# Performance work log

Hardware: AMD Instinct MI355X
Metric: run time of the kernel (lower is better)

## Reference

```python
import jax, jax.numpy as jnp
import numpy as np

NUM_NODES = 200000
NUM_EDGES = 600000
NUM_GRAPHS = 10000
BN_EPS = 1e-5


def setup_inputs() -> dict:
    key = jax.random.key(0)
    ks = jax.random.split(key, 10)
    x = jax.random.normal(ks[0], (NUM_NODES, 78), dtype=jnp.float32)
    edge_index = jax.random.randint(ks[1], (2, NUM_EDGES), 0, NUM_NODES, dtype=jnp.int64 if jax.config.jax_enable_x64 else jnp.int32)
    batch = jnp.sort(jax.random.randint(ks[2], (NUM_NODES,), 0, NUM_GRAPHS))
    def glorot(k, shape):
        fan_in, fan_out = shape[-2], shape[-1]
        s = jnp.sqrt(2.0 / (fan_in + fan_out))
        return jax.random.normal(k, shape, dtype=jnp.float32) * s
    return {
        "x": x,
        "edge_index": edge_index,
        "batch": batch,
        "W1_0": glorot(ks[3], (78, 128)),
        "b1_0": jnp.zeros((128,), jnp.float32),
        "W2_0": glorot(ks[4], (128, 128)),
        "b2_0": jnp.zeros((128,), jnp.float32),
        "g_0": jnp.ones((128,), jnp.float32),
        "be_0": jnp.zeros((128,), jnp.float32),
        "W1s": glorot(ks[5], (4, 128, 128)),
        "b1s": jnp.zeros((4, 128), jnp.float32),
        "W2s": glorot(ks[6], (4, 128, 128)),
        "b2s": jnp.zeros((4, 128), jnp.float32),
        "gs": jnp.ones((4, 128), jnp.float32),
        "bes": jnp.zeros((4, 128), jnp.float32),
        "fcW": glorot(ks[7], (128, 64)),
        "fcb": jnp.zeros((64,), jnp.float32),
    }


def _batchnorm(h, gamma, beta):
    # BatchNorm1d with batch statistics (training-mode normalization)
    mean = h.mean(axis=0)
    var = h.var(axis=0)  # biased, as torch uses for normalization
    return gamma * (h - mean) * jax.lax.rsqrt(var + BN_EPS) + beta


def _gin_block(h, src, dst, W1, b1, W2, b2, gamma, beta):
    # GINConv (eps=0): MLP(x + sum of neighbor messages), then ReLU + BN
    agg = jax.ops.segment_sum(h[src], dst, num_segments=NUM_NODES)  # [N, d]
    z = h + agg
    z = jax.nn.relu(z @ W1 + b1) @ W2 + b2
    z = jax.nn.relu(z)
    return _batchnorm(z, gamma, beta)


def reference(x, edge_index, batch, W1_0, b1_0, W2_0, b2_0, g_0, be_0,
              W1s, b1s, W2s, b2s, gs, bes, fcW, fcb):
    src, dst = edge_index[0], edge_index[1]
    h = _gin_block(x, src, dst, W1_0, b1_0, W2_0, b2_0, g_0, be_0)  # [N, 128]

    def body(h, params):
        W1, b1, W2, b2, g, be = params
        return _gin_block(h, src, dst, W1, b1, W2, b2, g, be), None

    h, _ = jax.lax.scan(body, h, (W1s, b1s, W2s, b2s, gs, bes))

    pooled = jax.ops.segment_sum(h, batch, num_segments=NUM_GRAPHS)  # [G, 128]
    out = jax.nn.relu(pooled @ fcW + fcb)  # [G, 64]; dropout is identity at eval
    return out
```

## Files before the change

### kernel.cpp

```cpp
#include <hip/hip_runtime.h>
#include <hip/hip_bf16.h>

#define NN 200000
#define NE 600000
#define NG 10000
#define NCH 98

typedef __attribute__((ext_vector_type(8))) short bfrag;
typedef __attribute__((ext_vector_type(4))) float f32x4;
typedef unsigned short u16;

static __device__ __forceinline__ u16 f2b(float x) {
  __hip_bfloat16 b = __float2bfloat16(x);
  return __builtin_bit_cast(u16, b);
}
static __device__ __forceinline__ float b2f(u16 u) {
  __hip_bfloat16 b = __builtin_bit_cast(__hip_bfloat16, u);
  return __bfloat162float(b);
}
static __device__ __forceinline__ void split(float v, u16& hi, u16& lo) {
  hi = f2b(v);
  lo = f2b(v - b2f(hi));
}

__global__ void prep_kernel(const float* __restrict__ W1_0, const float* __restrict__ W2_0,
                            const float* __restrict__ W1s, const float* __restrict__ W2s,
                            u16* __restrict__ wf) {
  int i = blockIdx.x * 256 + threadIdx.x;
  if (i >= 312 * 64) return;
  int t = i >> 6, lane = i & 63;
  const float* W;
  int KS, ct, kk, Krows, base, half;
  if (t < 24) {
    W = W1_0; KS = 3; ct = t / 3; kk = t - ct * 3; Krows = 78; base = 0; half = 12288;
  } else if (t < 56) {
    int u = t - 24;
    W = W2_0; KS = 4; ct = u >> 2; kk = u & 3; Krows = 128; base = 24576; half = 16384;
  } else {
    int u = t - 56;
    int j = u >> 6, r = u & 63;
    KS = 4; Krows = 128; half = 16384;
    if (r < 32) {
      W = W1s + j * 16384; ct = r >> 2; kk = r & 3; base = 57344 + j * 65536;
    } else {
      W = W2s + j * 16384; r -= 32; ct = r >> 2; kk = r & 3; base = 57344 + j * 65536 + 32768;
    }
  }
  int col = ct * 16 + (lane & 15);
  int idx = ((ct * KS + kk) * 64 + lane) * 8;
  for (int jj = 0; jj < 8; jj++) {
    int k = kk * 32 + 8 * (lane >> 4) + jj;
    float v = (k < Krows) ? W[k * 128 + col] : 0.f;
    u16 hi, lo;
    split(v, hi, lo);
    wf[base + idx + jj] = hi;
    wf[base + half + idx + jj] = lo;
  }
}

__global__ void hist_kernel(const int* __restrict__ dst, int* __restrict__ deg) {
  int e = blockIdx.x * 256 + threadIdx.x;
  if (e < NE) atomicAdd(&deg[dst[e]], 1);
}

__global__ void scan1_kernel(const int* __restrict__ deg, int* __restrict__ csum) {
  __shared__ int s[256];
  int base = blockIdx.x * 2048 + threadIdx.x * 8;
  int t = 0;
#pragma unroll
  for (int j = 0; j < 8; j++) {
    int idx = base + j;
    if (idx < NN) t += deg[idx];
  }
  s[threadIdx.x] = t;
  __syncthreads();
  for (int o = 128; o > 0; o >>= 1) {
    if (threadIdx.x < o) s[threadIdx.x] += s[threadIdx.x + o];
    __syncthreads();
  }
  if (threadIdx.x == 0) csum[blockIdx.x] = s[0];
}

__global__ void scan2_kernel(int* __restrict__ csum, int* __restrict__ rowptr) {
  int acc = 0;
  for (int i = 0; i < NCH; i++) {
    int v = csum[i];
    csum[i] = acc;
    acc += v;
  }
  rowptr[NN] = acc;
}

__global__ void scan3_kernel(const int* deg, const int* __restrict__ csum,
                             int* __restrict__ rowptr, int* cursor) {
  __shared__ int s[256];
  int tid = threadIdx.x;
  int base = blockIdx.x * 2048 + tid * 8;
  int loc[8];
  int t = 0;
#pragma unroll
  for (int j = 0; j < 8; j++) {
    int idx = base + j;
    int d = (idx < NN) ? deg[idx] : 0;
    loc[j] = t;
    t += d;
  }
  s[tid] = t;
  __syncthreads();
  for (int o = 1; o < 256; o <<= 1) {
    int u = (tid >= o) ? s[tid - o] : 0;
    __syncthreads();
    s[tid] += u;
    __syncthreads();
  }
  int off = csum[blockIdx.x] + s[tid] - t;
#pragma unroll
  for (int j = 0; j < 8; j++) {
    int idx = base + j;
    if (idx < NN) {
      int r = off + loc[j];
      rowptr[idx] = r;
      cursor[idx] = r;
    }
  }
}

__global__ void scatter_kernel(const int* __restrict__ src, const int* __restrict__ dst,
                               int* __restrict__ cursor, int* __restrict__ csr_src) {
  int e = blockIdx.x * 256 + threadIdx.x;
  if (e < NE) {
    int p = atomicAdd(&cursor[dst[e]], 1);
    csr_src[p] = src[e];
  }
}

template <bool FIRST>
__global__ __launch_bounds__(512, 4) void fused_kernel(
    const float* __restrict__ xin, const float* __restrict__ hin,
    const float* __restrict__ ss,
    const int* __restrict__ rowptr, const int* __restrict__ csr_src,
    const u16* __restrict__ w1hi, const u16* __restrict__ w1lo,
    const u16* __restrict__ w2hi, const u16* __restrict__ w2lo,
    const float* __restrict__ b1, const float* __restrict__ b2,
    float* __restrict__ hout, float* __restrict__ stats) {
  constexpr int KS1 = FIRST ? 3 : 4;
  constexpr int AH = 0, AL = 8704, TH = 17408, TL = 26112;
  __shared__ u16 lds[34816];
  const int tid = threadIdx.x;
  const int w = tid >> 6, l = tid & 63;
  const int l15 = l & 15, lg = l >> 4;
  const float bb1 = b1[w * 16 + l15];
  const float bb2 = b2[w * 16 + l15];
  float s_acc = 0.f, q_acc = 0.f;

  float4 sc4, sh4;
  if (!FIRST) {
    int k4 = (l & 31) * 4;
    sc4 = *reinterpret_cast<const float4*>(&ss[k4]);
    sh4 = *reinterpret_cast<const float4*>(&ss[128 + k4]);
  }

  for (int tile = blockIdx.x; tile < 3125; tile += gridDim.x) {
    const int rows0 = tile * 64;

    if (FIRST) {
      const float2* x2 = reinterpret_cast<const float2*>(xin);
      for (int j = 0; j < 8; j++) {
        int row = w * 8 + j;
        int node = rows0 + row;
        int beg = rowptr[node], end = rowptr[node + 1];
        int f0 = l * 2;
        if (f0 < 78) {
          size_t fid = (size_t)node * 39 + (f0 >> 1);
          float2 acc = x2[fid];
          int i = beg;
          for (; i + 1 < end; i += 2) {
            int s0 = csr_src[i], s1 = csr_src[i + 1];
            float2 v0 = x2[(size_t)s0 * 39 + (f0 >> 1)];
            float2 v1 = x2[(size_t)s1 * 39 + (f0 >> 1)];
            acc.x += v0.x + v1.x;
            acc.y += v0.y + v1.y;
          }
          if (i < end) {
            int s0 = csr_src[i];
            float2 v0 = x2[(size_t)s0 * 39 + (f0 >> 1)];
            acc.x += v0.x;
            acc.y += v0.y;
          }
          ushort2 oh, ol;
          split(acc.x, oh.x, ol.x);
          split(acc.y, oh.y, ol.y);
          *reinterpret_cast<ushort2*>(&lds[AH + row * 136 + f0]) = oh;
          *reinterpret_cast<ushort2*>(&lds[AL + row * 136 + f0]) = ol;
        } else if (f0 < 96) {
          ushort2 z = {0, 0};
          *reinterpret_cast<ushort2*>(&lds[AH + row * 136 + f0]) = z;
          *reinterpret_cast<ushort2*>(&lds[AL + row * 136 + f0]) = z;
        }
      }
    } else {
      const float4* h4p = reinterpret_cast<const float4*>(hin);
      int k4 = (l & 31) * 4;
      for (int p = 0; p < 4; p++) {
        int row = w * 8 + p * 2 + (l >> 5);
        int node = rows0 + row;
        int beg = rowptr[node], end = rowptr[node + 1];
        size_t foff = (size_t)(k4 >> 2);
        float4 acc = h4p[(size_t)node * 32 + foff];
        int i = beg;
        for (; i + 1 < end; i += 2) {
          int s0 = csr_src[i], s1 = csr_src[i + 1];
          float4 v0 = h4p[(size_t)s0 * 32 + foff];
          float4 v1 = h4p[(size_t)s1 * 32 + foff];
          acc.x += v0.x + v1.x;
          acc.y += v0.y + v1.y;
          acc.z += v0.z + v1.z;
          acc.w += v0.w + v1.w;
        }
        if (i < end) {
          int s0 = csr_src[i];
          float4 v0 = h4p[(size_t)s0 * 32 + foff];
          acc.x += v0.x;
          acc.y += v0.y;
          acc.z += v0.z;
          acc.w += v0.w;
        }
        float cnt = (float)(end - beg + 1);
        float a0 = acc.x * sc4.x + cnt * sh4.x;
        float a1 = acc.y * sc4.y + cnt * sh4.y;
        float a2 = acc.z * sc4.z + cnt * sh4.z;
        float a3 = acc.w * sc4.w + cnt * sh4.w;
        ushort4 oh, ol;
        split(a0, oh.x, ol.x);
        split(a1, oh.y, ol.y);
        split(a2, oh.z, ol.z);
        split(a3, oh.w, ol.w);
        *reinterpret_cast<ushort4*>(&lds[AH + row * 136 + k4]) = oh;
        *reinterpret_cast<ushort4*>(&lds[AL + row * 136 + k4]) = ol;
      }
    }
    bfrag w1h[KS1], w1l[KS1];
#pragma unroll
    for (int kk = 0; kk < KS1; kk++) {
      int fi = ((w * KS1 + kk) * 64 + l) * 8;
      w1h[kk] = *reinterpret_cast<const bfrag*>(&w1hi[fi]);
      w1l[kk] = *reinterpret_cast<const bfrag*>(&w1lo[fi]);
    }
    __syncthreads();

#pragma unroll
    for (int rt = 0; rt < 4; rt++) {
      f32x4 acc = {bb1, bb1, bb1, bb1};
      const int arow = (rt * 16 + l15) * 136 + 8 * lg;
#pragma unroll
      for (int kk = 0; kk < KS1; kk++) {
        bfrag ah = *reinterpret_cast<const bfrag*>(&lds[AH + arow + kk * 32]);
        bfrag al = *reinterpret_cast<const bfrag*>(&lds[AL + arow + kk * 32]);
        acc = __builtin_amdgcn_mfma_f32_16x16x32_bf16(al, w1h[kk], acc, 0, 0, 0);
        acc = __builtin_amdgcn_mfma_f32_16x16x32_bf16(ah, w1l[kk], acc, 0, 0, 0);
        acc = __builtin_amdgcn_mfma_f32_16x16x32_bf16(ah, w1h[kk], acc, 0, 0, 0);
      }
#pragma unroll
      for (int r = 0; r < 4; r++) {
        float v = fmaxf(acc[r], 0.f);
        u16 hi, lo;
        split(v, hi, lo);
        int off = (rt * 16 + 4 * lg + r) * 136 + w * 16 + l15;
        lds[TH + off] = hi;
        lds[TL + off] = lo;
      }
    }
    bfrag w2h[4], w2l[4];
#pragma unroll
    for (int kk = 0; kk < 4; kk++) {
      int fi = ((w * 4 + kk) * 64 + l) * 8;
      w2h[kk] = *reinterpret_cast<const bfrag*>(&w2hi[fi]);
      w2l[kk] = *reinterpret_cast<const bfrag*>(&w2lo[fi]);
    }
    __syncthreads();

#pragma unroll
    for (int rt = 0; rt < 4; rt++) {
      f32x4 acc = {bb2, bb2, bb2, bb2};
      const int arow = (rt * 16 + l15) * 136 + 8 * lg;
#pragma unroll
      for (int kk = 0; kk < 4; kk++) {
        bfrag th = *reinterpret_cast<const bfrag*>(&lds[TH + arow + kk * 32]);
        bfrag tl = *reinterpret_cast<const bfrag*>(&lds[TL + arow + kk * 32]);
        acc = __builtin_amdgcn_mfma_f32_16x16x32_bf16(tl, w2h[kk], acc, 0, 0, 0);
        acc = __builtin_amdgcn_mfma_f32_16x16x32_bf16(th, w2l[kk], acc, 0, 0, 0);
        acc = __builtin_amdgcn_mfma_f32_16x16x32_bf16(th, w2h[kk], acc, 0, 0, 0);
      }
#pragma unroll
      for (int r = 0; r < 4; r++) {
        float v = fmaxf(acc[r], 0.f);
        hout[(size_t)(rows0 + rt * 16 + 4 * lg + r) * 128 + w * 16 + l15] = v;
        s_acc += v;
        q_acc += v * v;
      }
    }
    __syncthreads();
  }
  s_acc += __shfl_xor(s_acc, 16);
  s_acc += __shfl_xor(s_acc, 32);
  q_acc += __shfl_xor(q_acc, 16);
  q_acc += __shfl_xor(q_acc, 32);
  if (lg == 0) {
    atomicAdd(&stats[w * 16 + l15], s_acc);
    atomicAdd(&stats[128 + w * 16 + l15], q_acc);
  }
}

__global__ void bn_kernel(const float* __restrict__ stats, const float* __restrict__ gamma,
                          const float* __restrict__ beta, float* __restrict__ ss) {
  int c = threadIdx.x;
  float mean = stats[c] * (1.f / NN);
  float var = stats[128 + c] * (1.f / NN) - mean * mean;
  var = fmaxf(var, 0.f);
  float sc = gamma[c] * rsqrtf(var + 1e-5f);
  ss[c] = sc;
  ss[128 + c] = beta[c] - mean * sc;
}

__global__ void pool_kernel(const float* __restrict__ h, const float* __restrict__ ss,
                            const int* __restrict__ batch, float* __restrict__ pooled) {
  int c = threadIdx.x;
  int n0 = blockIdx.x * 128;
  int n1 = min(n0 + 128, NN);
  float sc = ss[c], sh = ss[128 + c];
  float acc = 0.f;
  float cnt = 0.f;
  int gprev = batch[n0];
  for (int n = n0; n < n1; n++) {
    int g = batch[n];
    if (g != gprev) {
      atomicAdd(&pooled[gprev * 128 + c], sc * acc + cnt * sh);
      acc = 0.f;
      cnt = 0.f;
      gprev = g;
    }
    acc += h[(size_t)n * 128 + c];
    cnt += 1.f;
  }
  atomicAdd(&pooled[gprev * 128 + c], sc * acc + cnt * sh);
}

__global__ void fc_kernel(const float* __restrict__ pooled, const float* __restrict__ fcW,
                          const float* __restrict__ fcb, float* __restrict__ out) {
  int i = blockIdx.x * 256 + threadIdx.x;
  if (i >= NG * 64) return;
  int g = i >> 6, o = i & 63;
  float acc = fcb[o];
#pragma unroll 8
  for (int k = 0; k < 128; k++) acc += pooled[g * 128 + k] * fcW[k * 64 + o];
  out[i] = fmaxf(acc, 0.f);
}

extern "C" void kernel_launch(void* const* d_in, const int* in_sizes, int n_in,
                              void* d_out, int out_size, void* d_ws, size_t ws_size,
                              hipStream_t stream) {
  const float* x = (const float*)d_in[0];
  const int* ei = (const int*)d_in[1];
  const int* src = ei;
  const int* dst = ei + NE;
  const int* batch = (const int*)d_in[2];
  const float* W1_0 = (const float*)d_in[3];
  const float* b1_0 = (const float*)d_in[4];
  const float* W2_0 = (const float*)d_in[5];
  const float* b2_0 = (const float*)d_in[6];
  const float* g_0 = (const float*)d_in[7];
  const float* be_0 = (const float*)d_in[8];
  const float* W1s = (const float*)d_in[9];
  const float* b1s = (const float*)d_in[10];
  const float* W2s = (const float*)d_in[11];
  const float* b2s = (const float*)d_in[12];
  const float* gs = (const float*)d_in[13];
  const float* bes = (const float*)d_in[14];
  const float* fcW = (const float*)d_in[15];
  const float* fcb = (const float*)d_in[16];

  char* ws = (char*)d_ws;
  float* buf0 = (float*)(ws + 0);
  float* buf1 = (float*)(ws + 102400000);
  float* POOLED = (float*)(ws + 204800000);
  float* STATS = (float*)(ws + 209920000);
  float* SS = (float*)(ws + 209921024);
  u16* WF = (u16*)(ws + 209922048);
  int* ROWPTR = (int*)(ws + 210561024);
  int* CURSOR = (int*)(ws + 211361040);
  int* CSRC = (int*)(ws + 212161040);
  int* CSUM = (int*)(ws + 214561040);

  prep_kernel<<<78, 256, 0, stream>>>(W1_0, W2_0, W1s, W2s, WF);

  hipMemsetAsync(CURSOR, 0, NN * 4, stream);
  hist_kernel<<<(NE + 255) / 256, 256, 0, stream>>>(dst, CURSOR);
  scan1_kernel<<<NCH, 256, 0, stream>>>(CURSOR, CSUM);
  scan2_kernel<<<1, 1, 0, stream>>>(CSUM, ROWPTR);
  scan3_kernel<<<NCH, 256, 0, stream>>>(CURSOR, CSUM, ROWPTR, CURSOR);
  scatter_kernel<<<(NE + 255) / 256, 256, 0, stream>>>(src, dst, CURSOR, CSRC);

  float* buf[2] = {buf0, buf1};
  hipMemsetAsync(STATS, 0, 1024, stream);
  fused_kernel<true><<<512, 512, 0, stream>>>(x, nullptr, nullptr, ROWPTR, CSRC,
                                              WF, WF + 12288, WF + 24576, WF + 40960,
                                              b1_0, b2_0, buf0, STATS);
  bn_kernel<<<1, 128, 0, stream>>>(STATS, g_0, be_0, SS);

  for (int L = 1; L < 5; L++) {
    int j = L - 1;
    const float* hin = buf[(L + 1) & 1];
    float* hb = buf[L & 1];
    hipMemsetAsync(STATS, 0, 1024, stream);
    const u16* wl = WF + 57344 + j * 65536;
    fused_kernel<false><<<512, 512, 0, stream>>>(nullptr, hin, SS, ROWPTR, CSRC,
                                                 wl, wl + 16384, wl + 32768, wl + 49152,
                                                 b1s + j * 128, b2s + j * 128, hb, STATS);
    bn_kernel<<<1, 128, 0, stream>>>(STATS, gs + j * 128, bes + j * 128, SS);
  }

  hipMemsetAsync(POOLED, 0, (size_t)NG * 128 * 4, stream);
  pool_kernel<<<(NN + 127) / 128, 128, 0, stream>>>(buf[0], SS, batch, POOLED);
  fc_kernel<<<(NG * 64 + 255) / 256, 256, 0, stream>>>(POOLED, fcW, fcb, (float*)d_out);
}
```

Baseline: 752.8 us.

## Store intermediate node features in bf16 to halve gather and store traffic

Intermediate hidden states between GIN layers are now written as bf16 instead of fp32, and the neighbor gather reads 8-element bf16 vectors per lane with a 4-way unrolled edge loop. The pooling kernel reads bf16 too. This halves the memory traffic of the random-access gather and of the layer output writes, which dominate the fused kernel. The cost is lost precision in the stored activations: the hi/lo split for the matmul no longer recovers full fp32 inputs, so accuracy against the fp32 reference may degrade.

```diff
diff --git a/kernel.cpp b/kernel.cpp
--- a/kernel.cpp
+++ b/kernel.cpp
@@ -136,13 +136,13 @@
 
 template <bool FIRST>
 __global__ __launch_bounds__(512, 4) void fused_kernel(
-    const float* __restrict__ xin, const float* __restrict__ hin,
+    const float* __restrict__ xin, const u16* __restrict__ hin,
     const float* __restrict__ ss,
     const int* __restrict__ rowptr, const int* __restrict__ csr_src,
     const u16* __restrict__ w1hi, const u16* __restrict__ w1lo,
     const u16* __restrict__ w2hi, const u16* __restrict__ w2lo,
     const float* __restrict__ b1, const float* __restrict__ b2,
-    float* __restrict__ hout, float* __restrict__ stats) {
+    u16* __restrict__ hout, float* __restrict__ stats) {
   constexpr int KS1 = FIRST ? 3 : 4;
   constexpr int AH = 0, AL = 8704, TH = 17408, TL = 26112;
   __shared__ u16 lds[34816];
@@ -153,11 +153,14 @@
   const float bb2 = b2[w * 16 + l15];
   float s_acc = 0.f, q_acc = 0.f;
 
-  float4 sc4, sh4;
+  float sc8[8], sh8[8];
   if (!FIRST) {
-    int k4 = (l & 31) * 4;
-    sc4 = *reinterpret_cast<const float4*>(&ss[k4]);
-    sh4 = *reinterpret_cast<const float4*>(&ss[128 + k4]);
+    int k8 = l15 * 8;
+#pragma unroll
+    for (int j = 0; j < 8; j++) {
+      sc8[j] = ss[k8 + j];
+      sh8[j] = ss[128 + k8 + j];
+    }
   }
 
   for (int tile = blockIdx.x; tile < 3125; tile += gridDim.x) {
@@ -199,44 +202,46 @@
         }
       }
     } else {
-      const float4* h4p = reinterpret_cast<const float4*>(hin);
-      int k4 = (l & 31) * 4;
-      for (int p = 0; p < 4; p++) {
-        int row = w * 8 + p * 2 + (l >> 5);
+      const bfrag* hp = reinterpret_cast<const bfrag*>(hin);
+      const int k8v = l15;
+      for (int p = 0; p < 2; p++) {
+        int row = w * 8 + p * 4 + lg;
         int node = rows0 + row;
         int beg = rowptr[node], end = rowptr[node + 1];
-        size_t foff = (size_t)(k4 >> 2);
-        float4 acc = h4p[(size_t)node * 32 + foff];
+        float a[8];
+        bfrag vs = hp[(size_t)node * 16 + k8v];
+#pragma unroll
+        for (int j = 0; j < 8; j++) a[j] = b2f((u16)vs[j]);
         int i = beg;
-        for (; i + 1 < end; i += 2) {
+        for (; i + 3 < end; i += 4) {
           int s0 = csr_src[i], s1 = csr_src[i + 1];
-          float4 v0 = h4p[(size_t)s0 * 32 + foff];
-          float4 v1 = h4p[(size_t)s1 * 32 + foff];
-          acc.x += v0.x + v1.x;
-          acc.y += v0.y + v1.y;
-          acc.z += v0.z + v1.z;
-          acc.w += v0.w + v1.w;
+          int s2 = csr_src[i + 2], s3 = csr_src[i + 3];
+          bfrag v0 = hp[(size_t)s0 * 16 + k8v];
+          bfrag v1 = hp[(size_t)s1 * 16 + k8v];
+          bfrag v2 = hp[(size_t)s2 * 16 + k8v];
+          bfrag v3 = hp[(size_t)s3 * 16 + k8v];
+#pragma unroll
+          for (int j = 0; j < 8; j++)
+            a[j] += (b2f((u16)v0[j]) + b2f((u16)v1[j])) + (b2f((u16)v2[j]) + b2f((u16)v3[j]));
         }
-        if (i < end) {
+        for (; i < end; i++) {
           int s0 = csr_src[i];
-          float4 v0 = h4p[(size_t)s0 * 32 + foff];
-          acc.x += v0.x;
-          acc.y += v0.y;
-          acc.z += v0.z;
-          acc.w += v0.w;
+          bfrag v0 = hp[(size_t)s0 * 16 + k8v];
+#pragma unroll
+          for (int j = 0; j < 8; j++) a[j] += b2f((u16)v0[j]);
         }
         float cnt = (float)(end - beg + 1);
-        float a0 = acc.x * sc4.x + cnt * sh4.x;
-        float a1 = acc.y * sc4.y + cnt * sh4.y;
-        float a2 = acc.z * sc4.z + cnt * sh4.z;
-        float a3 = acc.w * sc4.w + cnt * sh4.w;
-        ushort4 oh, ol;
-        split(a0, oh.x, ol.x);
-        split(a1, oh.y, ol.y);
-        split(a2, oh.z, ol.z);
-        split(a3, oh.w, ol.w);
-        *reinterpret_cast<ushort4*>(&lds[AH + row * 136 + k4]) = oh;
-        *reinterpret_cast<ushort4*>(&lds[AL + row * 136 + k4]) = ol;
+        bfrag oh, ol;
+#pragma unroll
+        for (int j = 0; j < 8; j++) {
+          float t = a[j] * sc8[j] + cnt * sh8[j];
+          u16 hi, lo;
+          split(t, hi, lo);
+          oh[j] = (short)hi;
+          ol[j] = (short)lo;
+        }
+        *reinterpret_cast<bfrag*>(&lds[AH + row * 136 + l15 * 8]) = oh;
+        *reinterpret_cast<bfrag*>(&lds[AL + row * 136 + l15 * 8]) = ol;
       }
     }
     bfrag w1h[KS1], w1l[KS1];
@@ -294,7 +299,7 @@
 #pragma unroll
       for (int r = 0; r < 4; r++) {
         float v = fmaxf(acc[r], 0.f);
-        hout[(size_t)(rows0 + rt * 16 + 4 * lg + r) * 128 + w * 16 + l15] = v;
+        hout[(size_t)(rows0 + rt * 16 + 4 * lg + r) * 128 + w * 16 + l15] = f2b(v);
         s_acc += v;
         q_acc += v * v;
       }
@@ -322,7 +327,7 @@
   ss[128 + c] = beta[c] - mean * sc;
 }
 
-__global__ void pool_kernel(const float* __restrict__ h, const float* __restrict__ ss,
+__global__ void pool_kernel(const u16* __restrict__ h, const float* __restrict__ ss,
                             const int* __restrict__ batch, float* __restrict__ pooled) {
   int c = threadIdx.x;
   int n0 = blockIdx.x * 128;
@@ -339,7 +344,7 @@
       cnt = 0.f;
       gprev = g;
     }
-    acc += h[(size_t)n * 128 + c];
+    acc += b2f(h[(size_t)n * 128 + c]);
     cnt += 1.f;
   }
   atomicAdd(&pooled[gprev * 128 + c], sc * acc + cnt * sh);
@@ -380,16 +385,16 @@
   const float* fcb = (const float*)d_in[16];
 
   char* ws = (char*)d_ws;
-  float* buf0 = (float*)(ws + 0);
-  float* buf1 = (float*)(ws + 102400000);
-  float* POOLED = (float*)(ws + 204800000);
-  float* STATS = (float*)(ws + 209920000);
-  float* SS = (float*)(ws + 209921024);
-  u16* WF = (u16*)(ws + 209922048);
-  int* ROWPTR = (int*)(ws + 210561024);
-  int* CURSOR = (int*)(ws + 211361040);
-  int* CSRC = (int*)(ws + 212161040);
-  int* CSUM = (int*)(ws + 214561040);
+  u16* buf0 = (u16*)(ws + 0);
+  u16* buf1 = (u16*)(ws + 51200000);
+  float* POOLED = (float*)(ws + 102400000);
+  float* STATS = (float*)(ws + 107520000);
+  float* SS = (float*)(ws + 107521024);
+  u16* WF = (u16*)(ws + 107522048);
+  int* ROWPTR = (int*)(ws + 108161024);
+  int* CURSOR = (int*)(ws + 108961040);
+  int* CSRC = (int*)(ws + 109761040);
+  int* CSUM = (int*)(ws + 112161040);
 
   prep_kernel<<<78, 256, 0, stream>>>(W1_0, W2_0, W1s, W2s, WF);
 
@@ -400,7 +405,7 @@
   scan3_kernel<<<NCH, 256, 0, stream>>>(CURSOR, CSUM, ROWPTR, CURSOR);
   scatter_kernel<<<(NE + 255) / 256, 256, 0, stream>>>(src, dst, CURSOR, CSRC);
 
-  float* buf[2] = {buf0, buf1};
+  u16* buf[2] = {buf0, buf1};
   hipMemsetAsync(STATS, 0, 1024, stream);
   fused_kernel<true><<<512, 512, 0, stream>>>(x, nullptr, nullptr, ROWPTR, CSRC,
                                               WF, WF + 12288, WF + 24576, WF + 40960,
@@ -409,8 +414,8 @@
 
   for (int L = 1; L < 5; L++) {
     int j = L - 1;
-    const float* hin = buf[(L + 1) & 1];
-    float* hb = buf[L & 1];
+    const u16* hin = buf[(L + 1) & 1];
+    u16* hb = buf[L & 1];
     hipMemsetAsync(STATS, 0, 1024, stream);
     const u16* wl = WF + 57344 + j * 65536;
     fused_kernel<false><<<512, 512, 0, stream>>>(nullptr, hin, SS, ROWPTR, CSRC,
```

New measurement: 690.9 us. 8.2% less time.
